# Kernel optimization log

Measured on AMD Instinct MI355X. Metric: run time of the kernel, lower is better.

## Reference

```python
import jax, jax.numpy as jnp
import numpy as np

N, M, NBR = 20000, 12, 64
AF, ORIG, H, B, K = 256, 92, 256, 200, 50
N_CONV = 3
EPS = 1e-5


def _bn_train(x, gamma, beta):
    mu = x.mean(0)
    var = x.var(0)  # biased, matches torch BN normalization in train mode
    return (x - mu) * jax.lax.rsqrt(var + EPS) * gamma + beta


def _conv_layer(atom_in, nbr_fea, nbr_idx, w1, b1, w2, b2, gamma, beta):
    n, m = nbr_idx.shape
    m1 = m // 2
    atom_nbr = atom_in[nbr_idx]                     # [N, M, AF]
    atom_u = jnp.broadcast_to(atom_in[:, None, :], (n, m1, atom_in.shape[-1]))
    an1, an2 = atom_nbr[:, :m1], atom_nbr[:, m1:]
    nf1, nf2 = nbr_fea[:, :m1], nbr_fea[:, m1:]
    u1 = jnp.concatenate([atom_u, an1, nf1], axis=2)  # [N, M1, 2*AF+NBR]
    u2 = jnp.concatenate([atom_u, an2, nf2], axis=2)
    g1 = jax.nn.relu(jnp.einsum('nmf,fo->nmo', u1, w1) + b1)
    g2 = jax.nn.softplus(jnp.einsum('nmf,fo->nmo', u2, w1) + b1)
    nbr_sumed = g1.sum(1) + g2.sum(1)               # sum over all M neighbors, [N, 2*AF]
    nbr_sumed = nbr_sumed @ w2 + b2                 # [N, AF]
    nbr_sumed = _bn_train(nbr_sumed, gamma, beta)
    return jax.nn.softplus(atom_in + nbr_sumed)


def setup_inputs() -> dict:
    key = jax.random.key(0)
    ks = jax.random.split(key, 16)
    inp = {
        'atom_fea': jax.random.normal(ks[0], (N, ORIG), jnp.float32),
        'nbr_fea': jax.random.normal(ks[1], (N, M, NBR), jnp.float32),
        'nbr_fea_idx': jax.random.randint(ks[2], (N, M), 0, N),
        'M1_index': jax.random.randint(ks[3], (B * K,), 0, N),
        'seg_ids': jnp.repeat(jnp.arange(B), K),
        'm2_fea': jax.random.normal(ks[4], (B, 4), jnp.float32),
        'emb_w': jax.random.normal(ks[5], (ORIG, AF), jnp.float32) * 0.05,
        'emb_b': jnp.zeros((AF,), jnp.float32),
        'w1': jax.random.normal(ks[6], (N_CONV, 2 * AF + NBR, 2 * AF), jnp.float32) * 0.05,
        'b1': jnp.zeros((N_CONV, 2 * AF), jnp.float32),
        'w2': jax.random.normal(ks[7], (N_CONV, 2 * AF, AF), jnp.float32) * 0.05,
        'b2': jnp.zeros((N_CONV, AF), jnp.float32),
        'gamma': jnp.ones((N_CONV, AF), jnp.float32),
        'beta': jnp.zeros((N_CONV, AF), jnp.float32),
        'fc_w': jax.random.normal(ks[8], (AF + 4, H), jnp.float32) * 0.05,
        'fc_b': jnp.zeros((H,), jnp.float32),
        'out_w': jax.random.normal(ks[9], (H, 1), jnp.float32) * 0.05,
        'out_b': jnp.zeros((1,), jnp.float32),
    }
    return inp


def reference(atom_fea, nbr_fea, nbr_fea_idx, M1_index, seg_ids, m2_fea,
              emb_w, emb_b, w1, b1, w2, b2, gamma, beta,
              fc_w, fc_b, out_w, out_b):
    x = jax.nn.softplus(atom_fea @ emb_w + emb_b)           # [N, AF]
    for i in range(N_CONV):
        x = _conv_layer(x, nbr_fea, nbr_fea_idx, w1[i], b1[i], w2[i], b2[i], gamma[i], beta[i])
    m1_fea = x[M1_index]                                    # [B*K, AF]
    sums = jax.ops.segment_sum(m1_fea, seg_ids, num_segments=B)
    counts = jax.ops.segment_sum(jnp.ones((m1_fea.shape[0], 1), m1_fea.dtype), seg_ids, num_segments=B)
    crys = sums / counts                                    # per-crystal mean, [B, AF]
    crys = jnp.concatenate([crys, m2_fea], axis=1)          # [B, AF+4]
    h = jax.nn.softplus(jax.nn.softplus(crys) @ fc_w + fc_b)
    out = h @ out_w + out_b                                 # [B, 1]
    return out
```

## Files before the change

kernel.cpp:

```cpp
#include <hip/hip_runtime.h>
#include <hip/hip_bf16.h>


#define N_ATOM 20000
#define AF     256
#define F2     512
#define ORIG   92
#define ORIG_P 96
#define BB     200
#define KK     50
#define BN_EPS 1e-5f
#define ZS2    268

#define OFF_B1   0
#define OFF_B2   1536
#define OFF_GAM  2304
#define OFF_BET  3072
#define OFF_EMBB 3840
#define OFF_FCB  4096
#define OFF_FCW  4352
#define OFF_OW   70912
#define OFF_OB   71168
#define OFF_M2   71169
#define N_SMALL  71969

#define S_AF   (N_ATOM * ORIG_P)
#define S_EMB  (AF * ORIG_P)
#define S_W12  (3 * 1024 * 256)
#define S_W1F  (3 * 512 * 64)
#define S_W2   (3 * AF * F2)
#define S_SM   N_SMALL
#define S_TOT  (S_AF + S_EMB + S_W12 + S_W1F + S_W2 + S_SM)

using bf16x8 = __attribute__((ext_vector_type(8))) short;
using f32x4  = __attribute__((ext_vector_type(4))) float;

__device__ __forceinline__ float bf2f(__hip_bfloat16 v) { return __bfloat162float(v); }
__device__ __forceinline__ __hip_bfloat16 f2bf(float v) { return __float2bfloat16(v); }
__device__ __forceinline__ unsigned short f2bfbits(float f) {
    unsigned u = __float_as_uint(f);
    u += 0x7fffu + ((u >> 16) & 1u);
    return (unsigned short)(u >> 16);
}
__device__ __forceinline__ float bfbits2f(unsigned short u) {
    return __uint_as_float(((unsigned)u) << 16);
}
__device__ __forceinline__ float softplus_f(float x) {
    return fmaxf(x, 0.f) + __logf(1.f + __expf(-fabsf(x)));
}
__device__ __forceinline__ float ld_any(const void* p, long idx, bool isf32) {
    return isf32 ? ((const float*)p)[idx] : bf2f(((const __hip_bfloat16*)p)[idx]);
}

__global__ void detect_dtype(const unsigned* __restrict__ gamma_raw,
                             unsigned* __restrict__ flag) {
    unsigned u = gamma_raw[0];
    flag[0] = ((u & 0xFFFFu) == 0u) ? 1u : 0u;
}

__global__ __launch_bounds__(256) void prep_nf(const void* __restrict__ nf,
                                               const unsigned* __restrict__ dflag,
                                               unsigned* __restrict__ out) {
    bool isf32 = dflag[0] != 0u;
    int idx = blockIdx.x * 256 + threadIdx.x;
    if (idx >= N_ATOM * 12 * 64 / 4) return;
    if (isf32) {
        float4 v = ((const float4*)nf)[idx];
        out[idx * 2]     = (unsigned)f2bfbits(v.x) | ((unsigned)f2bfbits(v.y) << 16);
        out[idx * 2 + 1] = (unsigned)f2bfbits(v.z) | ((unsigned)f2bfbits(v.w) << 16);
    } else {
        ((uint2*)out)[idx] = ((const uint2*)nf)[idx];
    }
}

__global__ __launch_bounds__(256)
void prep_all(const void* af, const void* emb_w, const void* w1, const void* w2,
              const void* b1, const void* b2, const void* gam, const void* bet,
              const void* embb, const void* fcb, const void* fcw,
              const void* ow, const void* ob, const void* m2,
              const unsigned* __restrict__ dflag,
              __hip_bfloat16* __restrict__ af_pad, __hip_bfloat16* __restrict__ embT,
              __hip_bfloat16* __restrict__ w1T2, __hip_bfloat16* __restrict__ w1Tf,
              __hip_bfloat16* __restrict__ w2T, __hip_bfloat16* __restrict__ smalls) {
    bool isf32 = dflag[0] != 0u;
    int i = blockIdx.x * 256 + threadIdx.x;
    if (i < S_AF) {
        int r = i / ORIG_P, k = i - r * ORIG_P;
        af_pad[i] = (k < ORIG) ? f2bf(ld_any(af, (long)r * ORIG + k, isf32)) : f2bf(0.f);
        return;
    }
    i -= S_AF;
    if (i < S_EMB) {
        int n = i / ORIG_P, k = i - n * ORIG_P;
        embT[i] = (k < ORIG) ? f2bf(ld_any(emb_w, (long)k * AF + n, isf32)) : f2bf(0.f);
        return;
    }
    i -= S_EMB;
    if (i < S_W12) {
        int l = i / (1024 * 256); int rem = i - l * (1024 * 256);
        int c = rem / 256, k = rem - c * 256;
        long src = (c < 512) ? ((long)(l * 576 + k) * F2 + c)
                             : ((long)(l * 576 + 256 + k) * F2 + (c - 512));
        w1T2[i] = f2bf(ld_any(w1, src, isf32));
        return;
    }
    i -= S_W12;
    if (i < S_W1F) {
        int l = i / (512 * 64); int rem = i - l * (512 * 64);
        int c = rem / 64, k = rem - c * 64;
        w1Tf[i] = f2bf(ld_any(w1, (long)(l * 576 + 512 + k) * F2 + c, isf32));
        return;
    }
    i -= S_W1F;
    if (i < S_W2) {
        int l = i / (AF * F2); int rem = i - l * (AF * F2);
        int n = rem / F2, k = rem - n * F2;
        w2T[i] = f2bf(ld_any(w2, (long)(l * F2 + k) * AF + n, isf32));
        return;
    }
    i -= S_W2;
    if (i >= S_SM) return;
    float v;
    if      (i < OFF_B2)   v = ld_any(b1,   i - OFF_B1,  isf32);
    else if (i < OFF_GAM)  v = ld_any(b2,   i - OFF_B2,  isf32);
    else if (i < OFF_BET)  v = ld_any(gam,  i - OFF_GAM, isf32);
    else if (i < OFF_EMBB) v = ld_any(bet,  i - OFF_BET, isf32);
    else if (i < OFF_FCB)  v = ld_any(embb, i - OFF_EMBB,isf32);
    else if (i < OFF_OW)   v = (i < OFF_FCW) ? ld_any(fcb, i - OFF_FCB, isf32)
                                             : ld_any(fcw, i - OFF_FCW, isf32);
    else if (i < OFF_OB)   v = ld_any(ow,   i - OFF_OW,  isf32);
    else if (i < OFF_M2)   v = ld_any(ob,   i - OFF_OB,  isf32);
    else                   v = ld_any(m2,   i - OFF_M2,  isf32);
    smalls[i] = f2bf(v);
}

template <bool OUT_BF16>
__global__ __launch_bounds__(256)
void gemm_kernel(const __hip_bfloat16* __restrict__ A, int lda,
                 const __hip_bfloat16* __restrict__ BT, int ldb,
                 void* __restrict__ Cp, int M, int ldc, int K,
                 const __hip_bfloat16* __restrict__ bias, int act,
                 float* __restrict__ st) {
    __shared__ __align__(16) unsigned short sA[128 * 40];
    __shared__ __align__(16) unsigned short sB[128 * 40];
    __shared__ float sS[128], sS2[128];
    int tid  = threadIdx.x;
    int mt   = blockIdx.x, nt = blockIdx.y;
    int wave = tid >> 6, lane = tid & 63, q = lane >> 4, ln = lane & 15;
    int wr   = wave >> 1, wc = wave & 1;

    if (st && tid < 128) { sS[tid] = 0.f; sS2[tid] = 0.f; }

    f32x4 acc[4][4];
    for (int i = 0; i < 4; i++)
        for (int j = 0; j < 4; j++) acc[i][j] = (f32x4){0.f, 0.f, 0.f, 0.f};

    for (int k0 = 0; k0 < K; k0 += 32) {
        for (int i = tid; i < 512; i += 256) {
            int r = i >> 2, ch = i & 3;
            int row = mt * 128 + r;
            uint4 va = make_uint4(0u, 0u, 0u, 0u);
            if (row < M) va = *(const uint4*)(A + (size_t)row * lda + k0 + ch * 8);
            *(uint4*)(&sA[r * 40 + ch * 8]) = va;
            int n = nt * 128 + r;
            uint4 vb = *(const uint4*)(BT + (size_t)n * ldb + k0 + ch * 8);
            *(uint4*)(&sB[r * 40 + ch * 8]) = vb;
        }
        __syncthreads();
        bf16x8 af[4], bf[4];
        for (int i = 0; i < 4; i++)
            af[i] = *(const bf16x8*)(&sA[(wr * 64 + i * 16 + ln) * 40 + q * 8]);
        for (int j = 0; j < 4; j++)
            bf[j] = *(const bf16x8*)(&sB[(wc * 64 + j * 16 + ln) * 40 + q * 8]);
        for (int i = 0; i < 4; i++)
            for (int j = 0; j < 4; j++)
                acc[i][j] = __builtin_amdgcn_mfma_f32_16x16x32_bf16(af[i], bf[j], acc[i][j], 0, 0, 0);
        __syncthreads();
    }
    for (int j = 0; j < 4; j++) {
        int cl  = wc * 64 + j * 16 + ln;
        int col = nt * 128 + cl;
        float bv = bias ? bf2f(bias[col]) : 0.f;
        float ls = 0.f, ls2 = 0.f;
        for (int i = 0; i < 4; i++) {
            for (int r = 0; r < 4; r++) {
                int row = mt * 128 + wr * 64 + i * 16 + q * 4 + r;
                if (row >= M) continue;
                float v = acc[i][j][r] + bv;
                if (st) { ls += v; ls2 += v * v; }
                if (act == 1) v = softplus_f(v);
                if (OUT_BF16) ((__hip_bfloat16*)Cp)[(size_t)row * ldc + col] = f2bf(v);
                else          ((float*)Cp)[(size_t)row * ldc + col] = v;
            }
        }
        if (st) { atomicAdd(&sS[cl], ls); atomicAdd(&sS2[cl], ls2); }
    }
    if (st) {
        __syncthreads();
        if (tid < 128) {
            int col = nt * 128 + tid;
            atomicAdd(&st[col], sS[tid]);
            atomicAdd(&st[AF + col], sS2[tid]);
        }
    }
}

__global__ __launch_bounds__(256)
void conv_fused(const void* __restrict__ nf,
                const unsigned* __restrict__ dflag,
                int prepped,
                const int* __restrict__ nidx,
                const __hip_bfloat16* __restrict__ xay,
                const __hip_bfloat16* __restrict__ b1l,
                const __hip_bfloat16* __restrict__ w1TfL,
                __hip_bfloat16* __restrict__ ns)
{
    __shared__ __align__(16) unsigned short sNF[48 * 72];
    __shared__ __align__(16) unsigned short sZ[48 * ZS2];
    __shared__ int sIdx[48];

    int tid = threadIdx.x;
    int ab  = blockIdx.x * 4;

    if (prepped || dflag[0] == 0u) {
        const __hip_bfloat16* nfB = (const __hip_bfloat16*)nf;
        for (int i = tid; i < 48 * 8; i += 256) {
            int r = i >> 3, ch = i & 7;
            uint4 v = *(const uint4*)(nfB + (size_t)(ab * 12 + r) * 64 + ch * 8);
            *(uint4*)(&sNF[r * 72 + ch * 8]) = v;
        }
    } else {
        const float* nfF = (const float*)nf;
        for (int i = tid; i < 48 * 8; i += 256) {
            int r = i >> 3, ch = i & 7;
            const float* src = nfF + (size_t)(ab * 12 + r) * 64 + ch * 8;
            float4 v0 = *(const float4*)(src);
            float4 v1 = *(const float4*)(src + 4);
            unsigned short* d = &sNF[r * 72 + ch * 8];
            d[0] = f2bfbits(v0.x); d[1] = f2bfbits(v0.y);
            d[2] = f2bfbits(v0.z); d[3] = f2bfbits(v0.w);
            d[4] = f2bfbits(v1.x); d[5] = f2bfbits(v1.y);
            d[6] = f2bfbits(v1.z); d[7] = f2bfbits(v1.w);
        }
    }
    if (tid < 48) sIdx[tid] = nidx[ab * 12 + tid];
    __syncthreads();

    int wave = tid >> 6, lane = tid & 63, q = lane >> 4, ln = lane & 15;
    int c0 = wave * 32;
    int a = wave, half = lane >> 5, lc = lane & 31;
    int n = ab + a;
    int zc = half * 128 + lc * 4;

    for (int tp = 0; tp < 2; tp++) {
        if (tp) __syncthreads();
        for (int t2 = 0; t2 < 2; t2++) {
            int cb = (tp * 2 + t2) * 128;
            bf16x8 bfr[2][2];
            for (int c2 = 0; c2 < 2; c2++)
                for (int ks = 0; ks < 2; ks++)
                    bfr[c2][ks] = *(const bf16x8*)(w1TfL +
                        (size_t)(cb + c0 + c2 * 16 + ln) * 64 + ks * 32 + q * 8);
            f32x4 acc[3][2];
            for (int rt = 0; rt < 3; rt++)
                for (int c2 = 0; c2 < 2; c2++) acc[rt][c2] = (f32x4){0.f, 0.f, 0.f, 0.f};
            for (int rt = 0; rt < 3; rt++) {
                bf16x8 a0 = *(const bf16x8*)(&sNF[(rt * 16 + ln) * 72 + q * 8]);
                bf16x8 a1 = *(const bf16x8*)(&sNF[(rt * 16 + ln) * 72 + 32 + q * 8]);
                acc[rt][0] = __builtin_amdgcn_mfma_f32_16x16x32_bf16(a0, bfr[0][0], acc[rt][0], 0, 0, 0);
                acc[rt][0] = __builtin_amdgcn_mfma_f32_16x16x32_bf16(a1, bfr[0][1], acc[rt][0], 0, 0, 0);
                acc[rt][1] = __builtin_amdgcn_mfma_f32_16x16x32_bf16(a0, bfr[1][0], acc[rt][1], 0, 0, 0);
                acc[rt][1] = __builtin_amdgcn_mfma_f32_16x16x32_bf16(a1, bfr[1][1], acc[rt][1], 0, 0, 0);
            }
            for (int rt = 0; rt < 3; rt++)
                for (int c2 = 0; c2 < 2; c2++)
                    for (int r = 0; r < 4; r++)
                        sZ[(rt * 16 + q * 4 + r) * ZS2 + t2 * 128 + c0 + c2 * 16 + ln] =
                            f2bfbits(acc[rt][c2][r]);
        }
        __syncthreads();

        int gc = tp * 256 + zc;
        uint2 xau = *(const uint2*)(xay + (size_t)n * 1024 + gc);
        uint2 b1u = *(const uint2*)(b1l + gc);
        float xa0 = bfbits2f((unsigned short)(xau.x & 0xffff)) +
                    bfbits2f((unsigned short)(b1u.x & 0xffff));
        float xa1 = bfbits2f((unsigned short)(xau.x >> 16)) +
                    bfbits2f((unsigned short)(b1u.x >> 16));
        float xa2 = bfbits2f((unsigned short)(xau.y & 0xffff)) +
                    bfbits2f((unsigned short)(b1u.y & 0xffff));
        float xa3 = bfbits2f((unsigned short)(xau.y >> 16)) +
                    bfbits2f((unsigned short)(b1u.y >> 16));
        float r0 = 0.f, r1 = 0.f, r2 = 0.f, r3 = 0.f;
#pragma unroll
        for (int m = 0; m < 12; m++) {
            int gi = sIdx[a * 12 + m];
            uint2 zz = *(const uint2*)(&sZ[(a * 12 + m) * ZS2 + zc]);
            uint2 yy = *(const uint2*)(xay + (size_t)gi * 1024 + 512 + gc);
            float v0 = bfbits2f((unsigned short)(zz.x & 0xffff)) + xa0 +
                       bfbits2f((unsigned short)(yy.x & 0xffff));
            float v1 = bfbits2f((unsigned short)(zz.x >> 16)) + xa1 +
                       bfbits2f((unsigned short)(yy.x >> 16));
            float v2 = bfbits2f((unsigned short)(zz.y & 0xffff)) + xa2 +
                       bfbits2f((unsigned short)(yy.y & 0xffff));
            float v3 = bfbits2f((unsigned short)(zz.y >> 16)) + xa3 +
                       bfbits2f((unsigned short)(yy.y >> 16));
            if (m < 6) {
                v0 = fmaxf(v0, 0.f); v1 = fmaxf(v1, 0.f);
                v2 = fmaxf(v2, 0.f); v3 = fmaxf(v3, 0.f);
            } else {
                v0 = softplus_f(v0); v1 = softplus_f(v1);
                v2 = softplus_f(v2); v3 = softplus_f(v3);
            }
            r0 += v0; r1 += v1; r2 += v2; r3 += v3;
        }
        uint2 o;
        o.x = (unsigned)f2bfbits(r0) | ((unsigned)f2bfbits(r1) << 16);
        o.y = (unsigned)f2bfbits(r2) | ((unsigned)f2bfbits(r3) << 16);
        *(uint2*)(ns + (size_t)n * F2 + gc) = o;
    }
}

__global__ __launch_bounds__(256)
void bn_apply(const __hip_bfloat16* __restrict__ h2, const float* __restrict__ st,
              const __hip_bfloat16* __restrict__ x,
              const __hip_bfloat16* __restrict__ gamma,
              const __hip_bfloat16* __restrict__ beta,
              __hip_bfloat16* __restrict__ xo) {
    int i = (blockIdx.x * 256 + threadIdx.x) * 8;
    int c = i & 255;
    uint4 hv = *(const uint4*)(h2 + i);
    uint4 xv = *(const uint4*)(x + i);
    unsigned hw[4] = {hv.x, hv.y, hv.z, hv.w};
    unsigned xw[4] = {xv.x, xv.y, xv.z, xv.w};
    unsigned ow[4];
    float r[8];
#pragma unroll
    for (int k = 0; k < 8; k++) {
        int cc = c + k;
        float mu  = st[cc] * (1.f / 20000.f);
        float var = fmaxf(st[AF + cc] * (1.f / 20000.f) - mu * mu, 0.f);
        unsigned hh = hw[k >> 1], xx = xw[k >> 1];
        float h  = bfbits2f((unsigned short)((k & 1) ? (hh >> 16) : (hh & 0xffff)));
        float xf = bfbits2f((unsigned short)((k & 1) ? (xx >> 16) : (xx & 0xffff)));
        float t = (h - mu) * rsqrtf(var + BN_EPS) * bf2f(gamma[cc]) + bf2f(beta[cc]);
        r[k] = softplus_f(xf + t);
    }
#pragma unroll
    for (int k = 0; k < 4; k++)
        ow[k] = (unsigned)f2bfbits(r[2 * k]) | ((unsigned)f2bfbits(r[2 * k + 1]) << 16);
    *(uint4*)(xo + i) = make_uint4(ow[0], ow[1], ow[2], ow[3]);
}

__global__ __launch_bounds__(256)
void readout(const __hip_bfloat16* __restrict__ x, const int* __restrict__ m1,
             const __hip_bfloat16* __restrict__ smalls,
             const unsigned* __restrict__ dflag,
             void* __restrict__ outp) {
    __shared__ float sc[AF + 4];
    __shared__ float sred[4];
    bool isf32 = dflag[0] != 0u;
    int b = blockIdx.x, tid = threadIdx.x;
    float s = 0.f;
    for (int j = 0; j < KK; j++) {
        int row = m1[b * KK + j];
        s += bf2f(x[(size_t)row * AF + tid]);
    }
    sc[tid] = softplus_f(s * (1.f / (float)KK));
    if (tid < 4) sc[AF + tid] = softplus_f(bf2f(smalls[OFF_M2 + b * 4 + tid]));
    __syncthreads();
    float acc = bf2f(smalls[OFF_FCB + tid]);
    for (int k = 0; k < AF + 4; k++) acc += sc[k] * bf2f(smalls[OFF_FCW + k * 256 + tid]);
    float h = softplus_f(acc);
    float v = h * bf2f(smalls[OFF_OW + tid]);
    for (int off = 32; off > 0; off >>= 1) v += __shfl_down(v, off);
    if ((tid & 63) == 0) sred[tid >> 6] = v;
    __syncthreads();
    if (tid == 0) {
        float o = sred[0] + sred[1] + sred[2] + sred[3] + bf2f(smalls[OFF_OB]);
        if (isf32) ((float*)outp)[b] = o;
        else       ((__hip_bfloat16*)outp)[b] = f2bf(o);
    }
}

extern "C" void kernel_launch(void* const* d_in, const int* in_sizes, int n_in,
                              void* d_out, int out_size, void* d_ws, size_t ws_size,
                              hipStream_t stream) {
    const void* atom_fea = d_in[0];
    const void* nbr_fea  = d_in[1];
    const int*  nbr_idx  = (const int*)d_in[2];
    const int*  m1_idx   = (const int*)d_in[3];
    const void* m2_fea = d_in[5];
    const void* emb_w  = d_in[6];
    const void* emb_b  = d_in[7];
    const void* w1     = d_in[8];
    const void* b1     = d_in[9];
    const void* w2     = d_in[10];
    const void* b2     = d_in[11];
    const void* gamma  = d_in[12];
    const void* beta   = d_in[13];
    const void* fc_w   = d_in[14];
    const void* fc_b   = d_in[15];
    const void* out_w  = d_in[16];
    const void* out_b  = d_in[17];

    char* ws = (char*)d_ws;
    size_t off = 0;
    auto alloc = [&](size_t bytes) -> char* {
        char* p = ws + off;
        off += (bytes + 255) & ~(size_t)255;
        return p;
    };
    __hip_bfloat16* w1T2   = (__hip_bfloat16*)alloc((size_t)S_W12 * 2);
    __hip_bfloat16* w1Tf   = (__hip_bfloat16*)alloc((size_t)S_W1F * 2);
    __hip_bfloat16* w2T    = (__hip_bfloat16*)alloc((size_t)S_W2 * 2);
    __hip_bfloat16* smalls = (__hip_bfloat16*)alloc((size_t)N_SMALL * 2);
    __hip_bfloat16* xb0    = (__hip_bfloat16*)alloc((size_t)N_ATOM * AF * 2);
    __hip_bfloat16* xb1    = (__hip_bfloat16*)alloc((size_t)N_ATOM * AF * 2);
    char*           regXY  = alloc((size_t)N_ATOM * 1024 * 2);
    char*           regZ   = alloc((size_t)N_ATOM * F2 * 2);
    float*          stats  = (float*)alloc((size_t)3 * 2 * AF * 4);
    unsigned*       dflag  = (unsigned*)alloc(256);
    char*           nfb    = alloc((size_t)N_ATOM * 12 * 64 * 2);
    int use_nfb = (ws_size >= off) ? 1 : 0;

    __hip_bfloat16* xay    = (__hip_bfloat16*)regXY;
    __hip_bfloat16* h2     = (__hip_bfloat16*)regXY;
    __hip_bfloat16* af_pad = (__hip_bfloat16*)(regXY + (size_t)N_ATOM * F2 * 2);
    __hip_bfloat16* embT   = (__hip_bfloat16*)regZ;
    __hip_bfloat16* nsb    = (__hip_bfloat16*)regZ;

    detect_dtype<<<1, 1, 0, stream>>>((const unsigned*)gamma, dflag);
    (void)hipMemsetAsync(stats, 0, (size_t)3 * 2 * AF * 4, stream);

    if (use_nfb)
        prep_nf<<<(N_ATOM * 12 * 64 / 4 + 255) / 256, 256, 0, stream>>>(nbr_fea, dflag,
                                                                        (unsigned*)nfb);
    prep_all<<<(S_TOT + 255) / 256, 256, 0, stream>>>(
        atom_fea, emb_w, w1, w2, b1, b2, gamma, beta, emb_b, fc_b, fc_w,
        out_w, out_b, m2_fea, dflag, af_pad, embT, w1T2, w1Tf, w2T, smalls);

    dim3 g_emb((N_ATOM + 127) / 128, 2);
    gemm_kernel<true><<<g_emb, 256, 0, stream>>>(af_pad, ORIG_P, embT, ORIG_P,
                                                 xb0, N_ATOM, AF, ORIG_P,
                                                 smalls + OFF_EMBB, 1, nullptr);

    const void* nf_conv = use_nfb ? (const void*)nfb : nbr_fea;

    __hip_bfloat16* xc = xb0;
    __hip_bfloat16* xn = xb1;
    for (int l = 0; l < 3; l++) {
        dim3 gxy((N_ATOM + 127) / 128, 8);
        gemm_kernel<true><<<gxy, 256, 0, stream>>>(xc, AF, w1T2 + (size_t)l * 1024 * 256, 256,
                                                   xay, N_ATOM, 1024, AF, nullptr, 0, nullptr);
        conv_fused<<<N_ATOM / 4, 256, 0, stream>>>(nf_conv, dflag, use_nfb, nbr_idx, xay,
                                                   smalls + OFF_B1 + l * F2,
                                                   w1Tf + (size_t)l * 512 * 64, nsb);
        float* stl = stats + l * 2 * AF;
        dim3 gh2((N_ATOM + 127) / 128, 2);
        gemm_kernel<true><<<gh2, 256, 0, stream>>>(nsb, F2, w2T + (size_t)l * AF * F2, F2,
                                                   h2, N_ATOM, AF, F2,
                                                   smalls + OFF_B2 + l * AF, 0, stl);
        bn_apply<<<(N_ATOM * AF / 8) / 256, 256, 0, stream>>>(h2, stl, xc,
                                                              smalls + OFF_GAM + l * AF,
                                                              smalls + OFF_BET + l * AF, xn);
        __hip_bfloat16* t = xc; xc = xn; xn = t;
    }
    readout<<<BB, 256, 0, stream>>>(xc, m1_idx, smalls, dflag, d_out);
}
```

Measured before the change: 616.5 us.

## Store conv edge partials in fp32 LDS and reorder GEMM grid to N-major

The neighbor-feature MFMA in conv_fused swaps operand roles so each wave writes whole f32x4 rows straight into an fp32 LDS tile. This replaces the scattered per-element bf16 packing and lets the epilogue read float4 without unpacking, at the cost of roughly twice the LDS for that tile. Neighbor indices are hoisted into registers, and the bf16 unpack helpers are simplified to mask or shift operations. The GEMM grids are transposed so the column tiles that share an A row-block are launched next to each other, which is meant to improve L2 reuse of A.

Measured after the change: 678.5 us. 10.1% more time.

```diff
diff --git a/kernel.cpp b/kernel.cpp
--- a/kernel.cpp
+++ b/kernel.cpp
@@ -10,7 +10,7 @@
 #define BB     200
 #define KK     50
 #define BN_EPS 1e-5f
-#define ZS2    268
+#define ZSF    260
 
 #define OFF_B1   0
 #define OFF_B2   1536
@@ -42,9 +42,8 @@
     u += 0x7fffu + ((u >> 16) & 1u);
     return (unsigned short)(u >> 16);
 }
-__device__ __forceinline__ float bfbits2f(unsigned short u) {
-    return __uint_as_float(((unsigned)u) << 16);
-}
+__device__ __forceinline__ float bflo(unsigned u) { return __uint_as_float(u << 16); }
+__device__ __forceinline__ float bfhi(unsigned u) { return __uint_as_float(u & 0xffff0000u); }
 __device__ __forceinline__ float softplus_f(float x) {
     return fmaxf(x, 0.f) + __logf(1.f + __expf(-fabsf(x)));
 }
@@ -145,7 +144,7 @@
     __shared__ __align__(16) unsigned short sB[128 * 40];
     __shared__ float sS[128], sS2[128];
     int tid  = threadIdx.x;
-    int mt   = blockIdx.x, nt = blockIdx.y;
+    int nt   = blockIdx.x, mt = blockIdx.y;
     int wave = tid >> 6, lane = tid & 63, q = lane >> 4, ln = lane & 15;
     int wr   = wave >> 1, wc = wave & 1;
 
@@ -216,7 +215,7 @@
                 __hip_bfloat16* __restrict__ ns)
 {
     __shared__ __align__(16) unsigned short sNF[48 * 72];
-    __shared__ __align__(16) unsigned short sZ[48 * ZS2];
+    __shared__ __align__(16) float sZf[48 * ZSF];
     __shared__ int sIdx[48];
 
     int tid = threadIdx.x;
@@ -247,64 +246,48 @@
     __syncthreads();
 
     int wave = tid >> 6, lane = tid & 63, q = lane >> 4, ln = lane & 15;
-    int c0 = wave * 32;
-    int a = wave, half = lane >> 5, lc = lane & 31;
+    int a = wave;
     int n = ab + a;
-    int zc = half * 128 + lc * 4;
+    int gi[12];
+#pragma unroll
+    for (int m = 0; m < 12; m++) gi[m] = sIdx[a * 12 + m];
 
     for (int tp = 0; tp < 2; tp++) {
+        int cbase = tp * 256;
         if (tp) __syncthreads();
-        for (int t2 = 0; t2 < 2; t2++) {
-            int cb = (tp * 2 + t2) * 128;
-            bf16x8 bfr[2][2];
-            for (int c2 = 0; c2 < 2; c2++)
-                for (int ks = 0; ks < 2; ks++)
-                    bfr[c2][ks] = *(const bf16x8*)(w1TfL +
-                        (size_t)(cb + c0 + c2 * 16 + ln) * 64 + ks * 32 + q * 8);
-            f32x4 acc[3][2];
-            for (int rt = 0; rt < 3; rt++)
-                for (int c2 = 0; c2 < 2; c2++) acc[rt][c2] = (f32x4){0.f, 0.f, 0.f, 0.f};
+        int w0 = wave * 64;
+        for (int wt = 0; wt < 4; wt++) {
+            int wc = w0 + wt * 16;
+            bf16x8 afr0 = *(const bf16x8*)(w1TfL + (size_t)(cbase + wc + ln) * 64 + q * 8);
+            bf16x8 afr1 = *(const bf16x8*)(w1TfL + (size_t)(cbase + wc + ln) * 64 + 32 + q * 8);
             for (int rt = 0; rt < 3; rt++) {
-                bf16x8 a0 = *(const bf16x8*)(&sNF[(rt * 16 + ln) * 72 + q * 8]);
-                bf16x8 a1 = *(const bf16x8*)(&sNF[(rt * 16 + ln) * 72 + 32 + q * 8]);
-                acc[rt][0] = __builtin_amdgcn_mfma_f32_16x16x32_bf16(a0, bfr[0][0], acc[rt][0], 0, 0, 0);
-                acc[rt][0] = __builtin_amdgcn_mfma_f32_16x16x32_bf16(a1, bfr[0][1], acc[rt][0], 0, 0, 0);
-                acc[rt][1] = __builtin_amdgcn_mfma_f32_16x16x32_bf16(a0, bfr[1][0], acc[rt][1], 0, 0, 0);
-                acc[rt][1] = __builtin_amdgcn_mfma_f32_16x16x32_bf16(a1, bfr[1][1], acc[rt][1], 0, 0, 0);
+                bf16x8 b0 = *(const bf16x8*)(&sNF[(rt * 16 + ln) * 72 + q * 8]);
+                bf16x8 b1f = *(const bf16x8*)(&sNF[(rt * 16 + ln) * 72 + 32 + q * 8]);
+                f32x4 acc = (f32x4){0.f, 0.f, 0.f, 0.f};
+                acc = __builtin_amdgcn_mfma_f32_16x16x32_bf16(afr0, b0, acc, 0, 0, 0);
+                acc = __builtin_amdgcn_mfma_f32_16x16x32_bf16(afr1, b1f, acc, 0, 0, 0);
+                *(f32x4*)(&sZf[(rt * 16 + ln) * ZSF + wc + q * 4]) = acc;
             }
-            for (int rt = 0; rt < 3; rt++)
-                for (int c2 = 0; c2 < 2; c2++)
-                    for (int r = 0; r < 4; r++)
-                        sZ[(rt * 16 + q * 4 + r) * ZS2 + t2 * 128 + c0 + c2 * 16 + ln] =
-                            f2bfbits(acc[rt][c2][r]);
         }
         __syncthreads();
 
-        int gc = tp * 256 + zc;
+        int lc = lane * 4;
+        int gc = cbase + lc;
         uint2 xau = *(const uint2*)(xay + (size_t)n * 1024 + gc);
         uint2 b1u = *(const uint2*)(b1l + gc);
-        float xa0 = bfbits2f((unsigned short)(xau.x & 0xffff)) +
-                    bfbits2f((unsigned short)(b1u.x & 0xffff));
-        float xa1 = bfbits2f((unsigned short)(xau.x >> 16)) +
-                    bfbits2f((unsigned short)(b1u.x >> 16));
-        float xa2 = bfbits2f((unsigned short)(xau.y & 0xffff)) +
-                    bfbits2f((unsigned short)(b1u.y & 0xffff));
-        float xa3 = bfbits2f((unsigned short)(xau.y >> 16)) +
-                    bfbits2f((unsigned short)(b1u.y >> 16));
+        float xa0 = bflo(xau.x) + bflo(b1u.x);
+        float xa1 = bfhi(xau.x) + bfhi(b1u.x);
+        float xa2 = bflo(xau.y) + bflo(b1u.y);
+        float xa3 = bfhi(xau.y) + bfhi(b1u.y);
         float r0 = 0.f, r1 = 0.f, r2 = 0.f, r3 = 0.f;
 #pragma unroll
         for (int m = 0; m < 12; m++) {
-            int gi = sIdx[a * 12 + m];
-            uint2 zz = *(const uint2*)(&sZ[(a * 12 + m) * ZS2 + zc]);
-            uint2 yy = *(const uint2*)(xay + (size_t)gi * 1024 + 512 + gc);
-            float v0 = bfbits2f((unsigned short)(zz.x & 0xffff)) + xa0 +
-                       bfbits2f((unsigned short)(yy.x & 0xffff));
-            float v1 = bfbits2f((unsigned short)(zz.x >> 16)) + xa1 +
-                       bfbits2f((unsigned short)(yy.x >> 16));
-            float v2 = bfbits2f((unsigned short)(zz.y & 0xffff)) + xa2 +
-                       bfbits2f((unsigned short)(yy.y & 0xffff));
-            float v3 = bfbits2f((unsigned short)(zz.y >> 16)) + xa3 +
-                       bfbits2f((unsigned short)(yy.y >> 16));
+            float4 z = *(const float4*)(&sZf[(a * 12 + m) * ZSF + lc]);
+            uint2 yy = *(const uint2*)(xay + (size_t)gi[m] * 1024 + 512 + gc);
+            float v0 = z.x + xa0 + bflo(yy.x);
+            float v1 = z.y + xa1 + bfhi(yy.x);
+            float v2 = z.z + xa2 + bflo(yy.y);
+            float v3 = z.w + xa3 + bfhi(yy.y);
             if (m < 6) {
                 v0 = fmaxf(v0, 0.f); v1 = fmaxf(v1, 0.f);
                 v2 = fmaxf(v2, 0.f); v3 = fmaxf(v3, 0.f);
@@ -341,8 +324,8 @@
         float mu  = st[cc] * (1.f / 20000.f);
         float var = fmaxf(st[AF + cc] * (1.f / 20000.f) - mu * mu, 0.f);
         unsigned hh = hw[k >> 1], xx = xw[k >> 1];
-        float h  = bfbits2f((unsigned short)((k & 1) ? (hh >> 16) : (hh & 0xffff)));
-        float xf = bfbits2f((unsigned short)((k & 1) ? (xx >> 16) : (xx & 0xffff)));
+        float h  = (k & 1) ? bfhi(hh) : bflo(hh);
+        float xf = (k & 1) ? bfhi(xx) : bflo(xx);
         float t = (h - mu) * rsqrtf(var + BN_EPS) * bf2f(gamma[cc]) + bf2f(beta[cc]);
         r[k] = softplus_f(xf + t);
     }
@@ -440,7 +423,7 @@
         atom_fea, emb_w, w1, w2, b1, b2, gamma, beta, emb_b, fc_b, fc_w,
         out_w, out_b, m2_fea, dflag, af_pad, embT, w1T2, w1Tf, w2T, smalls);
 
-    dim3 g_emb((N_ATOM + 127) / 128, 2);
+    dim3 g_emb(2, (N_ATOM + 127) / 128);
     gemm_kernel<true><<<g_emb, 256, 0, stream>>>(af_pad, ORIG_P, embT, ORIG_P,
                                                  xb0, N_ATOM, AF, ORIG_P,
                                                  smalls + OFF_EMBB, 1, nullptr);
@@ -450,14 +433,14 @@
     __hip_bfloat16* xc = xb0;
     __hip_bfloat16* xn = xb1;
     for (int l = 0; l < 3; l++) {
-        dim3 gxy((N_ATOM + 127) / 128, 8);
+        dim3 gxy(8, (N_ATOM + 127) / 128);
         gemm_kernel<true><<<gxy, 256, 0, stream>>>(xc, AF, w1T2 + (size_t)l * 1024 * 256, 256,
                                                    xay, N_ATOM, 1024, AF, nullptr, 0, nullptr);
         conv_fused<<<N_ATOM / 4, 256, 0, stream>>>(nf_conv, dflag, use_nfb, nbr_idx, xay,
                                                    smalls + OFF_B1 + l * F2,
                                                    w1Tf + (size_t)l * 512 * 64, nsb);
         float* stl = stats + l * 2 * AF;
-        dim3 gh2((N_ATOM + 127) / 128, 2);
+        dim3 gh2(2, (N_ATOM + 127) / 128);
         gemm_kernel<true><<<gh2, 256, 0, stream>>>(nsb, F2, w2T + (size_t)l * AF * F2, F2,
                                                    h2, N_ATOM, AF, F2,
                                                    smalls + OFF_B2 + l * AF, 0, stl);
```
